# Performance work log

Measured on AMD Instinct MI355X. Metric: run time of the kernel, lower is better.

## Reference

```python
import jax, jax.numpy as jnp
import numpy as np

INT_MIN = jnp.iinfo(jnp.int32).min


def setup_inputs() -> dict:
    key = jax.random.key(0)
    ks = jax.random.split(key, 12)
    N, E, H, R, T = 200000, 100000, 100, 172, 100
    return {
        'src': jax.random.randint(ks[0], (E,), 0, N, dtype=jnp.int32),
        'dst': jax.random.randint(ks[1], (E,), 0, N, dtype=jnp.int32),
        't': jax.random.randint(ks[2], (E,), 0, 1000000, dtype=jnp.int32),
        'raw_msg': jax.random.normal(ks[3], (E, R), dtype=jnp.float32),
        'memory': jax.random.normal(ks[4], (N, H), dtype=jnp.float32),
        'last_update': jax.random.randint(ks[5], (N,), 0, 1000, dtype=jnp.int32),
        'te_w': jax.random.normal(ks[6], (T, 1), dtype=jnp.float32) * 0.1,
        'te_b': jax.random.normal(ks[7], (T,), dtype=jnp.float32) * 0.1,
        'w_ih': jax.random.normal(ks[8], (3 * H, 2 * H + R + T), dtype=jnp.float32) * 0.05,
        'w_hh': jax.random.normal(ks[9], (3 * H, H), dtype=jnp.float32) * 0.05,
        'b_ih': jax.random.normal(ks[10], (3 * H,), dtype=jnp.float32) * 0.05,
        'b_hh': jax.random.normal(ks[11], (3 * H,), dtype=jnp.float32) * 0.05,
    }


def reference(src, dst, t, raw_msg, memory, last_update, te_w, te_b, w_ih, w_hh, b_ih, b_hh):
    N, H = memory.shape
    E = src.shape[0]

    def time_enc(t_rel):  # Linear(1, time_dim) then cos, t_rel: [E] float
        return jnp.cos(t_rel[:, None] * te_w[:, 0][None, :] + te_b[None, :])

    # IdentityMessage: concat(mem[src], mem[dst], raw_msg, t_enc); two streams (s and d)
    t_enc_s = time_enc((t - last_update[src]).astype(raw_msg.dtype))
    t_enc_d = time_enc((t - last_update[dst]).astype(raw_msg.dtype))
    msg_s = jnp.concatenate([memory[src], memory[dst], raw_msg, t_enc_s], axis=-1)
    msg_d = jnp.concatenate([memory[dst], memory[src], raw_msg, t_enc_d], axis=-1)

    msg = jnp.concatenate([msg_s, msg_d], axis=0)        # [2E, msg_dim]
    idx = jnp.concatenate([src, dst], axis=0)            # [2E]
    t2 = jnp.concatenate([t, t], axis=0)                 # [2E]

    # LastAggregator: per node pick the message with maximum timestamp
    max_t = jnp.full((N,), INT_MIN, dtype=t2.dtype).at[idx].max(t2)
    cand = jnp.where(t2 == max_t[idx], jnp.arange(2 * E, dtype=jnp.int32), jnp.int32(-1))
    win = jnp.full((N,), -1, dtype=jnp.int32).at[idx].max(cand)  # winning edge per node
    has_msg = win >= 0
    aggr = jnp.where(has_msg[:, None], msg[jnp.clip(win, 0)], 0.0)  # [N, msg_dim]

    # GRUCell(msg_dim, H)
    gi = aggr @ w_ih.T + b_ih                             # [N, 3H]
    gh = memory @ w_hh.T + b_hh                           # [N, 3H]
    i_r, i_z, i_n = jnp.split(gi, 3, axis=-1)
    h_r, h_z, h_n = jnp.split(gh, 3, axis=-1)
    r = jax.nn.sigmoid(i_r + h_r)
    z = jax.nn.sigmoid(i_z + h_z)
    n = jnp.tanh(i_n + r * h_n)
    memory_new = (1.0 - z) * n + z * memory               # [N, H]

    last_update_new = last_update.at[idx].max(t2)         # scatter latest event time
    return memory_new, last_update_new
```

## Files before the change

### kernel.cpp

```cpp
#include <hip/hip_runtime.h>
#include <math.h>

typedef __attribute__((ext_vector_type(8))) short  short8;
typedef __attribute__((ext_vector_type(4))) float  f32x4;

static constexpr int H     = 100;
static constexpr int RD    = 172;
static constexpr int WK    = 472;
static constexpr int KTOT  = 640;
static constexpr int NKS   = 20;
static constexpr int CH    = 80;
static constexpr int MB    = 32;
static constexpr int GRPS  = 2;
static constexpr int BLK   = 448;
static constexpr int SLOTS = 64;
static constexpr int NTT   = 28;
static constexpr int BPK_N = NTT * NKS * 64 * 8;

__device__ inline unsigned short f2bf(float x) {
    union { float f; unsigned u; } v; v.f = x;
    return (unsigned short)((v.u + 0x7FFFu + ((v.u >> 16) & 1u)) >> 16);
}
__device__ inline f32x4 mfma16(short8 a, short8 b, f32x4 c) {
    return __builtin_amdgcn_mfma_f32_16x16x32_bf16(a, b, c, 0, 0, 0);
}
__device__ inline float4 ld4g(const float* base, int lc, int limit) {
    if (lc + 4 <= limit) return *(const float4*)(base + lc);
    return make_float4(0.f, 0.f, 0.f, 0.f);
}

__global__ __launch_bounds__(256) void k_init(int* __restrict__ maxt, int* __restrict__ win, int N) {
    int i = blockIdx.x * blockDim.x + threadIdx.x;
    if (i < N) { maxt[i] = (int)0x80000000; win[i] = -1; }
}

__global__ __launch_bounds__(256) void k_maxt(const int* __restrict__ src, const int* __restrict__ dst,
                                              const int* __restrict__ t, int* __restrict__ maxt, int E) {
    int j = blockIdx.x * blockDim.x + threadIdx.x;
    if (j < E) {
        int tj = t[j];
        atomicMax(&maxt[src[j]], tj);
        atomicMax(&maxt[dst[j]], tj);
    }
}

__global__ __launch_bounds__(256) void k_win(const int* __restrict__ src, const int* __restrict__ dst,
                                             const int* __restrict__ t, const int* __restrict__ maxt,
                                             int* __restrict__ win, int E) {
    int j = blockIdx.x * blockDim.x + threadIdx.x;
    if (j < E) {
        int tj = t[j];
        int s = src[j], d = dst[j];
        if (maxt[s] == tj) atomicMax(&win[s], j);
        if (maxt[d] == tj) atomicMax(&win[d], j + E);
    }
}

__global__ __launch_bounds__(256) void k_lu(const int* __restrict__ last_update, const int* __restrict__ maxt,
                                            float* __restrict__ out_lu, int N) {
    int i = blockIdx.x * blockDim.x + threadIdx.x;
    if (i < N) {
        int m = maxt[i], lu = last_update[i];
        out_lu[i] = (float)(m > lu ? m : lu);
    }
}

__global__ __launch_bounds__(256) void k_prep(const float* __restrict__ w_ih, const float* __restrict__ w_hh,
                                              unsigned short* __restrict__ B) {
    int idx = blockIdx.x * 256 + threadIdx.x;
    if (idx >= BPK_N) return;
    int jj   = idx & 7;
    int lane = (idx >> 3) & 63;
    int rest = idx >> 9;
    int ks   = rest % NKS;
    int tile = rest / NKS;
    int kk   = ks * 32 + ((lane >> 4) << 3) + jj;
    float v = 0.f;
    if (tile < 21) {
        int gate = tile / 7;
        int tcol = (tile % 7) * 16 + (lane & 15);
        if (tcol < 100) {
            if (kk < 512) {
                int col = -1;
                if (kk < 100)                   col = kk;
                else if (kk >= 104 && kk < 204) col = kk - 4;
                else if (kk >= 208 && kk < 380) col = kk - 8;
                else if (kk >= 384 && kk < 484) col = kk - 12;
                if (col >= 0) v = w_ih[(gate * 100 + tcol) * WK + col];
            } else {
                int khh = kk - 512;
                if (gate < 2 && khh < 100)
                    v = w_hh[(gate * 100 + tcol) * H + khh];
            }
        }
    } else {
        int tcol = (tile - 21) * 16 + (lane & 15);
        int khh  = kk - 512;
        if (tcol < 100 && khh >= 0 && khh < 100)
            v = w_hh[(200 + tcol) * H + khh];
    }
    B[idx] = f2bf(v);
}

__global__ __launch_bounds__(BLK, 6) void k_gru(
    const int* __restrict__ src, const int* __restrict__ dst, const int* __restrict__ t,
    const float* __restrict__ raw_msg, const float* __restrict__ memory,
    const int* __restrict__ last_update, const float* __restrict__ te_w,
    const float* __restrict__ te_b, const float* __restrict__ b_ih,
    const float* __restrict__ b_hh, const int* __restrict__ win,
    const unsigned short* __restrict__ Bpack,
    float* __restrict__ out_mem, int E, int N)
{
    __shared__ unsigned short sA[GRPS * NKS * SLOTS * 8];
    __shared__ int   s_other[MB];
    __shared__ int   s_j[MB];
    __shared__ int   s_has[MB];
    __shared__ float s_dt[MB];

    const int tid   = threadIdx.x;
    const int node0 = blockIdx.x * MB;

    if (tid < MB) {
        int node = node0 + tid;
        int w = win[node];
        int has = 0, j = 0, other = 0; float dt = 0.f;
        if (w >= 0) {
            has = 1;
            int e = (w < E) ? w : (w - E);
            j = e;
            other = (w < E) ? dst[e] : src[e];
            dt = (float)(t[e] - last_update[node]);
        }
        s_j[tid] = j; s_other[tid] = other; s_has[tid] = has; s_dt[tid] = dt;
    }
    __syncthreads();

    {
        const int nl    = tid & 31;
        const int node  = node0 + nl;
        const int has   = s_has[nl];
        const int other = s_other[nl];
        const int jw    = s_j[nl];
        const float dt  = s_dt[nl];
        const float* memN = memory + (size_t)node * H;
        const float* memO = memory + (size_t)other * H;
        const float* rawJ = raw_msg + (size_t)jw * RD;
        const int grp = nl >> 4;
        const int row = nl & 15;

        for (int c = tid >> 5; c < CH; c += BLK / 32) {
            const int kb = c * 8;
            float4 va = make_float4(0.f, 0.f, 0.f, 0.f), vb = va;
            if (kb < 512) {
                if (has) {
                    if (kb < 104)      { va = ld4g(memN, kb,       100); vb = ld4g(memN, kb + 4,   100); }
                    else if (kb < 208) { va = ld4g(memO, kb - 104, 100); vb = ld4g(memO, kb - 100, 100); }
                    else if (kb < 384) { va = ld4g(rawJ, kb - 208, RD ); vb = ld4g(rawJ, kb - 204, RD ); }
                    else {
                        const int lc = kb - 384;
                        float vv[8];
#pragma unroll
                        for (int q = 0; q < 8; ++q) {
                            int col = lc + q;
                            vv[q] = (col < 100) ? __cosf(fmaf(dt, te_w[col], te_b[col])) : 0.f;
                        }
                        va = make_float4(vv[0], vv[1], vv[2], vv[3]);
                        vb = make_float4(vv[4], vv[5], vv[6], vv[7]);
                    }
                }
            } else {
                va = ld4g(memN, kb - 512, 100);
                vb = ld4g(memN, kb - 508, 100);
            }
            short8 sv;
            sv[0] = (short)f2bf(va.x); sv[1] = (short)f2bf(va.y);
            sv[2] = (short)f2bf(va.z); sv[3] = (short)f2bf(va.w);
            sv[4] = (short)f2bf(vb.x); sv[5] = (short)f2bf(vb.y);
            sv[6] = (short)f2bf(vb.z); sv[7] = (short)f2bf(vb.w);
            const int ks  = c >> 2, sub = c & 3;
            const int slot = sub * 16 + (row ^ (sub << 2));
            *(short8*)&sA[((grp * NKS + ks) * SLOTS + slot) * 8] = sv;
        }
    }
    __syncthreads();

    const int wv    = tid >> 6;
    const int lane  = tid & 63;
    const int lrow  = lane & 15;
    const int lhi   = lane >> 4;
    const int slotl = lhi * 16 + (lrow ^ (lhi << 2));

    f32x4 ar[GRPS], az[GRPS], an[GRPS], ah[GRPS];
#pragma unroll
    for (int m = 0; m < GRPS; ++m) { ar[m] = (f32x4)0.f; az[m] = (f32x4)0.f; an[m] = (f32x4)0.f; ah[m] = (f32x4)0.f; }

    __builtin_amdgcn_s_setprio(1);
#pragma unroll
    for (int ks = 0; ks < NKS; ++ks) {
        short8 a0 = *(const short8*)&sA[((0 * NKS + ks) * SLOTS + slotl) * 8];
        short8 a1 = *(const short8*)&sA[((1 * NKS + ks) * SLOTS + slotl) * 8];
        short8 br = *(const short8*)&Bpack[(((size_t)(     wv) * NKS + ks) * 64 + lane) * 8];
        short8 bz = *(const short8*)&Bpack[(((size_t)( 7 + wv) * NKS + ks) * 64 + lane) * 8];
        short8 bn = (ks < 16)
                  ? *(const short8*)&Bpack[(((size_t)(14 + wv) * NKS + ks) * 64 + lane) * 8]
                  : *(const short8*)&Bpack[(((size_t)(21 + wv) * NKS + ks) * 64 + lane) * 8];
        ar[0] = mfma16(a0, br, ar[0]);  ar[1] = mfma16(a1, br, ar[1]);
        az[0] = mfma16(a0, bz, az[0]);  az[1] = mfma16(a1, bz, az[1]);
        if (ks < 16) { an[0] = mfma16(a0, bn, an[0]);  an[1] = mfma16(a1, bn, an[1]); }
        else         { ah[0] = mfma16(a0, bn, ah[0]);  ah[1] = mfma16(a1, bn, ah[1]); }
    }
    __builtin_amdgcn_s_setprio(0);

    const int c = wv * 16 + lrow;
    if (c < 100) {
        const float br_ = b_ih[c]       + b_hh[c];
        const float bz_ = b_ih[c + 100] + b_hh[c + 100];
        const float bin = b_ih[c + 200];
        const float bhn = b_hh[c + 200];
#pragma unroll
        for (int m = 0; m < GRPS; ++m) {
#pragma unroll
            for (int r = 0; r < 4; ++r) {
                const int node = node0 + m * 16 + lhi * 4 + r;
                const float h  = memory[(size_t)node * H + c];
                const float rg = 1.f / (1.f + __expf(-(ar[m][r] + br_)));
                const float zg = 1.f / (1.f + __expf(-(az[m][r] + bz_)));
                const float ng = tanhf(an[m][r] + bin + rg * (ah[m][r] + bhn));
                out_mem[(size_t)node * H + c] = (1.f - zg) * ng + zg * h;
            }
        }
    }
}

extern "C" void kernel_launch(void* const* d_in, const int* in_sizes, int n_in,
                              void* d_out, int out_size, void* d_ws, size_t ws_size,
                              hipStream_t stream)
{
    const int*   src         = (const int*)d_in[0];
    const int*   dst         = (const int*)d_in[1];
    const int*   t           = (const int*)d_in[2];
    const float* raw_msg     = (const float*)d_in[3];
    const float* memory      = (const float*)d_in[4];
    const int*   last_update = (const int*)d_in[5];
    const float* te_w        = (const float*)d_in[6];
    const float* te_b        = (const float*)d_in[7];
    const float* w_ih        = (const float*)d_in[8];
    const float* w_hh        = (const float*)d_in[9];
    const float* b_ih        = (const float*)d_in[10];
    const float* b_hh        = (const float*)d_in[11];

    const int E = in_sizes[0];
    const int N = in_sizes[5];

    float* out    = (float*)d_out;
    float* out_lu = out + (size_t)N * H;

    int* maxt = (int*)d_ws;
    int* win  = maxt + N;
    unsigned short* Bpack = (unsigned short*)(win + N);

    k_init<<<(N + 255) / 256, 256, 0, stream>>>(maxt, win, N);
    k_prep<<<(BPK_N + 255) / 256, 256, 0, stream>>>(w_ih, w_hh, Bpack);
    k_maxt<<<(E + 255) / 256, 256, 0, stream>>>(src, dst, t, maxt, E);
    k_win <<<(E + 255) / 256, 256, 0, stream>>>(src, dst, t, maxt, win, E);
    k_lu  <<<(N + 255) / 256, 256, 0, stream>>>(last_update, maxt, out_lu, N);
    k_gru <<<N / MB, BLK, 0, stream>>>(src, dst, t, raw_msg, memory, last_update,
                                       te_w, te_b, b_ih, b_hh, win, Bpack, out, E, N);
}
```

Baseline: 202.3 us.

## Load node memory once, reuse it for aggr and epilogue; widen blocks to 48 rows

Each block now covers 48 nodes (three 16-row MFMA groups) instead of 32, so every B-fragment load feeds more MFMAs. Each node's memory row is loaded from global memory only once. It is staged as bf16 in the hidden-state slots, copied under a has-message mask into the aggregated-message slots, and read back from shared memory for the GRU blend instead of going to global memory again. The change also packs bf16 conversion with v_cvt_pk_bf16_f32, replaces tanhf with an exp-based formula, and adds bounds checks for a partial last block. The costs are a larger LDS footprint (lower occupancy, launch bounds cut to 3) and the previous hidden state in the final blend now carries bf16 precision, which adds error to the output.

Measured after the change: 211.2 us. 4.4% more time.

```diff
diff --git a/kernel.cpp b/kernel.cpp
--- a/kernel.cpp
+++ b/kernel.cpp
@@ -9,9 +9,8 @@
 static constexpr int WK    = 472;
 static constexpr int KTOT  = 640;
 static constexpr int NKS   = 20;
-static constexpr int CH    = 80;
-static constexpr int MB    = 32;
-static constexpr int GRPS  = 2;
+static constexpr int MB    = 48;
+static constexpr int GRPS  = 3;
 static constexpr int BLK   = 448;
 static constexpr int SLOTS = 64;
 static constexpr int NTT   = 28;
@@ -20,6 +19,15 @@
 __device__ inline unsigned short f2bf(float x) {
     union { float f; unsigned u; } v; v.f = x;
     return (unsigned short)((v.u + 0x7FFFu + ((v.u >> 16) & 1u)) >> 16);
+}
+__device__ inline float bf2f(unsigned short b) {
+    union { unsigned u; float f; } v; v.u = ((unsigned)b) << 16;
+    return v.f;
+}
+__device__ inline unsigned pkbf(float a, float b) {
+    unsigned r;
+    asm("v_cvt_pk_bf16_f32 %0, %1, %2" : "=v"(r) : "v"(a), "v"(b));
+    return r;
 }
 __device__ inline f32x4 mfma16(short8 a, short8 b, f32x4 c) {
     return __builtin_amdgcn_mfma_f32_16x16x32_bf16(a, b, c, 0, 0, 0);
@@ -102,7 +110,7 @@
     B[idx] = f2bf(v);
 }
 
-__global__ __launch_bounds__(BLK, 6) void k_gru(
+__global__ __launch_bounds__(BLK, 3) void k_gru(
     const int* __restrict__ src, const int* __restrict__ dst, const int* __restrict__ t,
     const float* __restrict__ raw_msg, const float* __restrict__ memory,
     const int* __restrict__ last_update, const float* __restrict__ te_w,
@@ -122,40 +130,42 @@
 
     if (tid < MB) {
         int node = node0 + tid;
-        int w = win[node];
         int has = 0, j = 0, other = 0; float dt = 0.f;
-        if (w >= 0) {
-            has = 1;
-            int e = (w < E) ? w : (w - E);
-            j = e;
-            other = (w < E) ? dst[e] : src[e];
-            dt = (float)(t[e] - last_update[node]);
+        if (node < N) {
+            int w = win[node];
+            if (w >= 0) {
+                has = 1;
+                int e = (w < E) ? w : (w - E);
+                j = e;
+                other = (w < E) ? dst[e] : src[e];
+                dt = (float)(t[e] - last_update[node]);
+            }
         }
         s_j[tid] = j; s_other[tid] = other; s_has[tid] = has; s_dt[tid] = dt;
     }
     __syncthreads();
 
-    {
-        const int nl    = tid & 31;
+    if (tid < 384) {
+        const int nl    = tid % 48;
+        const int c0    = tid / 48;
         const int node  = node0 + nl;
+        const bool valid = node < N;
         const int has   = s_has[nl];
-        const int other = s_other[nl];
-        const int jw    = s_j[nl];
+        const float* memN = memory + (size_t)node * H;
+        const float* memO = memory + (size_t)s_other[nl] * H;
+        const float* rawJ = raw_msg + (size_t)s_j[nl] * RD;
         const float dt  = s_dt[nl];
-        const float* memN = memory + (size_t)node * H;
-        const float* memO = memory + (size_t)other * H;
-        const float* rawJ = raw_msg + (size_t)jw * RD;
         const int grp = nl >> 4;
         const int row = nl & 15;
 
-        for (int c = tid >> 5; c < CH; c += BLK / 32) {
+        for (int cc = c0; cc < 67; cc += 8) {
+            const int c  = cc + 13;
             const int kb = c * 8;
             float4 va = make_float4(0.f, 0.f, 0.f, 0.f), vb = va;
-            if (kb < 512) {
+            if (c < 64) {
                 if (has) {
-                    if (kb < 104)      { va = ld4g(memN, kb,       100); vb = ld4g(memN, kb + 4,   100); }
-                    else if (kb < 208) { va = ld4g(memO, kb - 104, 100); vb = ld4g(memO, kb - 100, 100); }
-                    else if (kb < 384) { va = ld4g(rawJ, kb - 208, RD ); vb = ld4g(rawJ, kb - 204, RD ); }
+                    if (c < 26)      { va = ld4g(memO, kb - 104, 100); vb = ld4g(memO, kb - 100, 100); }
+                    else if (c < 48) { va = ld4g(rawJ, kb - 208, RD ); vb = ld4g(rawJ, kb - 204, RD ); }
                     else {
                         const int lc = kb - 384;
                         float vv[8];
@@ -168,18 +178,29 @@
                         vb = make_float4(vv[4], vv[5], vv[6], vv[7]);
                     }
                 }
-            } else {
+            } else if (valid) {
                 va = ld4g(memN, kb - 512, 100);
                 vb = ld4g(memN, kb - 508, 100);
             }
-            short8 sv;
-            sv[0] = (short)f2bf(va.x); sv[1] = (short)f2bf(va.y);
-            sv[2] = (short)f2bf(va.z); sv[3] = (short)f2bf(va.w);
-            sv[4] = (short)f2bf(vb.x); sv[5] = (short)f2bf(vb.y);
-            sv[6] = (short)f2bf(vb.z); sv[7] = (short)f2bf(vb.w);
-            const int ks  = c >> 2, sub = c & 3;
-            const int slot = sub * 16 + (row ^ (sub << 2));
-            *(short8*)&sA[((grp * NKS + ks) * SLOTS + slot) * 8] = sv;
+            int4 sv;
+            sv.x = (int)pkbf(va.x, va.y);
+            sv.y = (int)pkbf(va.z, va.w);
+            sv.z = (int)pkbf(vb.x, vb.y);
+            sv.w = (int)pkbf(vb.z, vb.w);
+            {
+                const int ks = c >> 2, sub = c & 3;
+                const int slot = sub * 16 + (row ^ (sub << 2));
+                *(int4*)&sA[((grp * NKS + ks) * SLOTS + slot) * 8] = sv;
+            }
+            if (c >= 64 && c < 77) {
+                int4 sm_;
+                sm_.x = has ? sv.x : 0; sm_.y = has ? sv.y : 0;
+                sm_.z = has ? sv.z : 0; sm_.w = has ? sv.w : 0;
+                const int cm = c - 64;
+                const int ks = cm >> 2, sub = cm & 3;
+                const int slot = sub * 16 + (row ^ (sub << 2));
+                *(int4*)&sA[((grp * NKS + ks) * SLOTS + slot) * 8] = sm_;
+            }
         }
     }
     __syncthreads();
@@ -199,15 +220,16 @@
     for (int ks = 0; ks < NKS; ++ks) {
         short8 a0 = *(const short8*)&sA[((0 * NKS + ks) * SLOTS + slotl) * 8];
         short8 a1 = *(const short8*)&sA[((1 * NKS + ks) * SLOTS + slotl) * 8];
+        short8 a2 = *(const short8*)&sA[((2 * NKS + ks) * SLOTS + slotl) * 8];
         short8 br = *(const short8*)&Bpack[(((size_t)(     wv) * NKS + ks) * 64 + lane) * 8];
         short8 bz = *(const short8*)&Bpack[(((size_t)( 7 + wv) * NKS + ks) * 64 + lane) * 8];
         short8 bn = (ks < 16)
                   ? *(const short8*)&Bpack[(((size_t)(14 + wv) * NKS + ks) * 64 + lane) * 8]
                   : *(const short8*)&Bpack[(((size_t)(21 + wv) * NKS + ks) * 64 + lane) * 8];
-        ar[0] = mfma16(a0, br, ar[0]);  ar[1] = mfma16(a1, br, ar[1]);
-        az[0] = mfma16(a0, bz, az[0]);  az[1] = mfma16(a1, bz, az[1]);
-        if (ks < 16) { an[0] = mfma16(a0, bn, an[0]);  an[1] = mfma16(a1, bn, an[1]); }
-        else         { ah[0] = mfma16(a0, bn, ah[0]);  ah[1] = mfma16(a1, bn, ah[1]); }
+        ar[0] = mfma16(a0, br, ar[0]);  ar[1] = mfma16(a1, br, ar[1]);  ar[2] = mfma16(a2, br, ar[2]);
+        az[0] = mfma16(a0, bz, az[0]);  az[1] = mfma16(a1, bz, az[1]);  az[2] = mfma16(a2, bz, az[2]);
+        if (ks < 16) { an[0] = mfma16(a0, bn, an[0]);  an[1] = mfma16(a1, bn, an[1]);  an[2] = mfma16(a2, bn, an[2]); }
+        else         { ah[0] = mfma16(a0, bn, ah[0]);  ah[1] = mfma16(a1, bn, ah[1]);  ah[2] = mfma16(a2, bn, ah[2]); }
     }
     __builtin_amdgcn_s_setprio(0);
 
@@ -217,16 +239,25 @@
         const float bz_ = b_ih[c + 100] + b_hh[c + 100];
         const float bin = b_ih[c + 200];
         const float bhn = b_hh[c + 200];
+        const int ksh = 16 + (c >> 5);
+        const int sbh = (c >> 3) & 3;
+        const int ceh = c & 7;
 #pragma unroll
         for (int m = 0; m < GRPS; ++m) {
 #pragma unroll
             for (int r = 0; r < 4; ++r) {
                 const int node = node0 + m * 16 + lhi * 4 + r;
-                const float h  = memory[(size_t)node * H + c];
-                const float rg = 1.f / (1.f + __expf(-(ar[m][r] + br_)));
-                const float zg = 1.f / (1.f + __expf(-(az[m][r] + bz_)));
-                const float ng = tanhf(an[m][r] + bin + rg * (ah[m][r] + bhn));
-                out_mem[(size_t)node * H + c] = (1.f - zg) * ng + zg * h;
+                if (node < N) {
+                    const int rw   = lhi * 4 + r;
+                    const int slot = sbh * 16 + (rw ^ (sbh << 2));
+                    const float h  = bf2f(sA[((m * NKS + ksh) * SLOTS + slot) * 8 + ceh]);
+                    const float rg = 1.f / (1.f + __expf(-(ar[m][r] + br_)));
+                    const float zg = 1.f / (1.f + __expf(-(az[m][r] + bz_)));
+                    const float xn = an[m][r] + bin + rg * (ah[m][r] + bhn);
+                    const float ex = __expf(2.f * fabsf(xn));
+                    const float th = copysignf(1.f - 2.f / (ex + 1.f), xn);
+                    out_mem[(size_t)node * H + c] = (1.f - zg) * th + zg * h;
+                }
             }
         }
     }
@@ -264,6 +295,6 @@
     k_maxt<<<(E + 255) / 256, 256, 0, stream>>>(src, dst, t, maxt, E);
     k_win <<<(E + 255) / 256, 256, 0, stream>>>(src, dst, t, maxt, win, E);
     k_lu  <<<(N + 255) / 256, 256, 0, stream>>>(last_update, maxt, out_lu, N);
-    k_gru <<<N / MB, BLK, 0, stream>>>(src, dst, t, raw_msg, memory, last_update,
-                                       te_w, te_b, b_ih, b_hh, win, Bpack, out, E, N);
-}
+    k_gru <<<(N + MB - 1) / MB, BLK, 0, stream>>>(src, dst, t, raw_msg, memory, last_update,
+                                                  te_w, te_b, b_ih, b_hh, win, Bpack, out, E, N);
+}
```

## Load GRU A-operands directly from global into registers, drop LDS staging

Applied to the files above, without the earlier changes.

The GRU kernel no longer stages the gathered message rows through shared memory with two barriers. Each of the 7 waves now loads its own A-fragments straight from global memory, using per-node pointers that fall back to a zero buffer for nodes without a message. The block grows from 32 to 48 nodes (3 MFMA groups) to amortise the B-weight loads. Other changes: bf16 conversion uses the packed v_cvt_pk_bf16_f32 instruction, tanh uses an exp-based formula, and tail blocks get bounds checks. The cost is that every wave re-reads the same gathered rows and recomputes the cosines redundantly, and register pressure rises.

Result: slower. 385.3 us (+90.4%).

```diff
diff --git a/kernel.cpp b/kernel.cpp
--- a/kernel.cpp
+++ b/kernel.cpp
@@ -7,20 +7,23 @@
 static constexpr int H     = 100;
 static constexpr int RD    = 172;
 static constexpr int WK    = 472;
-static constexpr int KTOT  = 640;
 static constexpr int NKS   = 20;
-static constexpr int CH    = 80;
-static constexpr int MB    = 32;
-static constexpr int GRPS  = 2;
+static constexpr int MB    = 48;
+static constexpr int GRPS  = 3;
 static constexpr int BLK   = 448;
-static constexpr int SLOTS = 64;
 static constexpr int NTT   = 28;
 static constexpr int BPK_N = NTT * NKS * 64 * 8;
+static constexpr int ZBF   = 256;
 
 __device__ inline unsigned short f2bf(float x) {
     union { float f; unsigned u; } v; v.f = x;
     return (unsigned short)((v.u + 0x7FFFu + ((v.u >> 16) & 1u)) >> 16);
 }
+__device__ inline unsigned pkbf(float a, float b) {
+    unsigned r;
+    asm("v_cvt_pk_bf16_f32 %0, %1, %2" : "=v"(r) : "v"(a), "v"(b));
+    return r;
+}
 __device__ inline f32x4 mfma16(short8 a, short8 b, f32x4 c) {
     return __builtin_amdgcn_mfma_f32_16x16x32_bf16(a, b, c, 0, 0, 0);
 }
@@ -29,9 +32,11 @@
     return make_float4(0.f, 0.f, 0.f, 0.f);
 }
 
-__global__ __launch_bounds__(256) void k_init(int* __restrict__ maxt, int* __restrict__ win, int N) {
+__global__ __launch_bounds__(256) void k_init(int* __restrict__ maxt, int* __restrict__ win,
+                                              float* __restrict__ zbuf, int N) {
     int i = blockIdx.x * blockDim.x + threadIdx.x;
     if (i < N) { maxt[i] = (int)0x80000000; win[i] = -1; }
+    if (i < ZBF) zbuf[i] = 0.f;
 }
 
 __global__ __launch_bounds__(256) void k_maxt(const int* __restrict__ src, const int* __restrict__ dst,
@@ -102,114 +107,99 @@
     B[idx] = f2bf(v);
 }
 
-__global__ __launch_bounds__(BLK, 6) void k_gru(
+__global__ __launch_bounds__(BLK) void k_gru(
     const int* __restrict__ src, const int* __restrict__ dst, const int* __restrict__ t,
     const float* __restrict__ raw_msg, const float* __restrict__ memory,
     const int* __restrict__ last_update, const float* __restrict__ te_w,
     const float* __restrict__ te_b, const float* __restrict__ b_ih,
     const float* __restrict__ b_hh, const int* __restrict__ win,
-    const unsigned short* __restrict__ Bpack,
+    const unsigned short* __restrict__ Bpack, const float* __restrict__ zbuf,
     float* __restrict__ out_mem, int E, int N)
 {
-    __shared__ unsigned short sA[GRPS * NKS * SLOTS * 8];
-    __shared__ int   s_other[MB];
-    __shared__ int   s_j[MB];
-    __shared__ int   s_has[MB];
-    __shared__ float s_dt[MB];
-
     const int tid   = threadIdx.x;
-    const int node0 = blockIdx.x * MB;
-
-    if (tid < MB) {
-        int node = node0 + tid;
-        int w = win[node];
-        int has = 0, j = 0, other = 0; float dt = 0.f;
-        if (w >= 0) {
-            has = 1;
-            int e = (w < E) ? w : (w - E);
-            j = e;
-            other = (w < E) ? dst[e] : src[e];
-            dt = (float)(t[e] - last_update[node]);
-        }
-        s_j[tid] = j; s_other[tid] = other; s_has[tid] = has; s_dt[tid] = dt;
-    }
-    __syncthreads();
-
-    {
-        const int nl    = tid & 31;
-        const int node  = node0 + nl;
-        const int has   = s_has[nl];
-        const int other = s_other[nl];
-        const int jw    = s_j[nl];
-        const float dt  = s_dt[nl];
-        const float* memN = memory + (size_t)node * H;
-        const float* memO = memory + (size_t)other * H;
-        const float* rawJ = raw_msg + (size_t)jw * RD;
-        const int grp = nl >> 4;
-        const int row = nl & 15;
-
-        for (int c = tid >> 5; c < CH; c += BLK / 32) {
-            const int kb = c * 8;
-            float4 va = make_float4(0.f, 0.f, 0.f, 0.f), vb = va;
-            if (kb < 512) {
-                if (has) {
-                    if (kb < 104)      { va = ld4g(memN, kb,       100); vb = ld4g(memN, kb + 4,   100); }
-                    else if (kb < 208) { va = ld4g(memO, kb - 104, 100); vb = ld4g(memO, kb - 100, 100); }
-                    else if (kb < 384) { va = ld4g(rawJ, kb - 208, RD ); vb = ld4g(rawJ, kb - 204, RD ); }
-                    else {
-                        const int lc = kb - 384;
-                        float vv[8];
-#pragma unroll
-                        for (int q = 0; q < 8; ++q) {
-                            int col = lc + q;
-                            vv[q] = (col < 100) ? __cosf(fmaf(dt, te_w[col], te_b[col])) : 0.f;
-                        }
-                        va = make_float4(vv[0], vv[1], vv[2], vv[3]);
-                        vb = make_float4(vv[4], vv[5], vv[6], vv[7]);
-                    }
-                }
-            } else {
-                va = ld4g(memN, kb - 512, 100);
-                vb = ld4g(memN, kb - 508, 100);
-            }
-            short8 sv;
-            sv[0] = (short)f2bf(va.x); sv[1] = (short)f2bf(va.y);
-            sv[2] = (short)f2bf(va.z); sv[3] = (short)f2bf(va.w);
-            sv[4] = (short)f2bf(vb.x); sv[5] = (short)f2bf(vb.y);
-            sv[6] = (short)f2bf(vb.z); sv[7] = (short)f2bf(vb.w);
-            const int ks  = c >> 2, sub = c & 3;
-            const int slot = sub * 16 + (row ^ (sub << 2));
-            *(short8*)&sA[((grp * NKS + ks) * SLOTS + slot) * 8] = sv;
-        }
-    }
-    __syncthreads();
-
     const int wv    = tid >> 6;
     const int lane  = tid & 63;
     const int lrow  = lane & 15;
-    const int lhi   = lane >> 4;
-    const int slotl = lhi * 16 + (lrow ^ (lhi << 2));
+    const int q     = lane >> 4;
+    const int node0 = blockIdx.x * MB;
+
+    const float* pN[GRPS];
+    const float* pM[GRPS];
+    const float* pO[GRPS];
+    const float* pR[GRPS];
+    float hasf[GRPS], dtv[GRPS];
+#pragma unroll
+    for (int g = 0; g < GRPS; ++g) {
+        const int node  = node0 + g * 16 + lrow;
+        const bool valid = node < N;
+        int w = valid ? win[node] : -1;
+        const bool has = (w >= 0);
+        int other = 0, jj = 0; float dt = 0.f;
+        if (has) {
+            const int lu = last_update[node];
+            const int e  = (w < E) ? w : (w - E);
+            jj    = e;
+            other = (w < E) ? dst[e] : src[e];
+            dt    = (float)(t[e] - lu);
+        }
+        pN[g]   = valid ? memory + (size_t)node * H : zbuf;
+        pM[g]   = has ? memory + (size_t)node * H : zbuf;
+        pO[g]   = has ? memory + (size_t)other * H : zbuf;
+        pR[g]   = has ? raw_msg + (size_t)jj * RD : zbuf;
+        hasf[g] = has ? 1.f : 0.f;
+        dtv[g]  = dt;
+    }
 
     f32x4 ar[GRPS], az[GRPS], an[GRPS], ah[GRPS];
 #pragma unroll
     for (int m = 0; m < GRPS; ++m) { ar[m] = (f32x4)0.f; az[m] = (f32x4)0.f; an[m] = (f32x4)0.f; ah[m] = (f32x4)0.f; }
 
-    __builtin_amdgcn_s_setprio(1);
 #pragma unroll
     for (int ks = 0; ks < NKS; ++ks) {
-        short8 a0 = *(const short8*)&sA[((0 * NKS + ks) * SLOTS + slotl) * 8];
-        short8 a1 = *(const short8*)&sA[((1 * NKS + ks) * SLOTS + slotl) * 8];
+        short8 a[GRPS];
+#pragma unroll
+        for (int g = 0; g < GRPS; ++g) {
+            const int k0 = ks * 32 + q * 8;
+            float4 fa, fb;
+            if (ks >= 12 && ks < 16) {
+                const int lc = k0 - 384;
+                const float4 w0 = ld4g(te_w, lc, 100), w1 = ld4g(te_w, lc + 4, 100);
+                const float4 c0 = ld4g(te_b, lc, 100), c1 = ld4g(te_b, lc + 4, 100);
+                const float hf = hasf[g], dt = dtv[g];
+                fa.x = hf * __cosf(fmaf(dt, w0.x, c0.x));
+                fa.y = hf * __cosf(fmaf(dt, w0.y, c0.y));
+                fa.z = hf * __cosf(fmaf(dt, w0.z, c0.z));
+                fa.w = hf * __cosf(fmaf(dt, w0.w, c0.w));
+                fb.x = hf * __cosf(fmaf(dt, w1.x, c1.x));
+                fb.y = hf * __cosf(fmaf(dt, w1.y, c1.y));
+                fb.z = hf * __cosf(fmaf(dt, w1.z, c1.z));
+                fb.w = hf * __cosf(fmaf(dt, w1.w, c1.w));
+            } else {
+                const float* base; int off, lim;
+                if (k0 < 104)      { base = pM[g]; off = k0;       lim = 100; }
+                else if (k0 < 208) { base = pO[g]; off = k0 - 104; lim = 100; }
+                else if (k0 < 384) { base = pR[g]; off = k0 - 208; lim = 172; }
+                else               { base = pN[g]; off = k0 - 512; lim = 100; }
+                fa = ld4g(base, off, lim);
+                fb = ld4g(base, off + 4, lim);
+            }
+            union { int4 i; short8 s; } u;
+            u.i.x = (int)pkbf(fa.x, fa.y);
+            u.i.y = (int)pkbf(fa.z, fa.w);
+            u.i.z = (int)pkbf(fb.x, fb.y);
+            u.i.w = (int)pkbf(fb.z, fb.w);
+            a[g] = u.s;
+        }
         short8 br = *(const short8*)&Bpack[(((size_t)(     wv) * NKS + ks) * 64 + lane) * 8];
         short8 bz = *(const short8*)&Bpack[(((size_t)( 7 + wv) * NKS + ks) * 64 + lane) * 8];
         short8 bn = (ks < 16)
                   ? *(const short8*)&Bpack[(((size_t)(14 + wv) * NKS + ks) * 64 + lane) * 8]
                   : *(const short8*)&Bpack[(((size_t)(21 + wv) * NKS + ks) * 64 + lane) * 8];
-        ar[0] = mfma16(a0, br, ar[0]);  ar[1] = mfma16(a1, br, ar[1]);
-        az[0] = mfma16(a0, bz, az[0]);  az[1] = mfma16(a1, bz, az[1]);
-        if (ks < 16) { an[0] = mfma16(a0, bn, an[0]);  an[1] = mfma16(a1, bn, an[1]); }
-        else         { ah[0] = mfma16(a0, bn, ah[0]);  ah[1] = mfma16(a1, bn, ah[1]); }
-    }
-    __builtin_amdgcn_s_setprio(0);
+        ar[0] = mfma16(a[0], br, ar[0]);  ar[1] = mfma16(a[1], br, ar[1]);  ar[2] = mfma16(a[2], br, ar[2]);
+        az[0] = mfma16(a[0], bz, az[0]);  az[1] = mfma16(a[1], bz, az[1]);  az[2] = mfma16(a[2], bz, az[2]);
+        if (ks < 16) { an[0] = mfma16(a[0], bn, an[0]);  an[1] = mfma16(a[1], bn, an[1]);  an[2] = mfma16(a[2], bn, an[2]); }
+        else         { ah[0] = mfma16(a[0], bn, ah[0]);  ah[1] = mfma16(a[1], bn, ah[1]);  ah[2] = mfma16(a[2], bn, ah[2]); }
+    }
 
     const int c = wv * 16 + lrow;
     if (c < 100) {
@@ -221,12 +211,16 @@
         for (int m = 0; m < GRPS; ++m) {
 #pragma unroll
             for (int r = 0; r < 4; ++r) {
-                const int node = node0 + m * 16 + lhi * 4 + r;
-                const float h  = memory[(size_t)node * H + c];
-                const float rg = 1.f / (1.f + __expf(-(ar[m][r] + br_)));
-                const float zg = 1.f / (1.f + __expf(-(az[m][r] + bz_)));
-                const float ng = tanhf(an[m][r] + bin + rg * (ah[m][r] + bhn));
-                out_mem[(size_t)node * H + c] = (1.f - zg) * ng + zg * h;
+                const int node = node0 + m * 16 + q * 4 + r;
+                if (node < N) {
+                    const float h  = memory[(size_t)node * H + c];
+                    const float rg = 1.f / (1.f + __expf(-(ar[m][r] + br_)));
+                    const float zg = 1.f / (1.f + __expf(-(az[m][r] + bz_)));
+                    const float xn = an[m][r] + bin + rg * (ah[m][r] + bhn);
+                    const float ex = __expf(2.f * fabsf(xn));
+                    const float th = copysignf(1.f - 2.f / (ex + 1.f), xn);
+                    out_mem[(size_t)node * H + c] = (1.f - zg) * th + zg * h;
+                }
             }
         }
     }
@@ -258,12 +252,16 @@
     int* maxt = (int*)d_ws;
     int* win  = maxt + N;
     unsigned short* Bpack = (unsigned short*)(win + N);
-
-    k_init<<<(N + 255) / 256, 256, 0, stream>>>(maxt, win, N);
+    float* zbuf = (float*)(Bpack + BPK_N);
+
+    const int nblk = (N + MB - 1) / MB;
+
+    k_init<<<(N + 255) / 256, 256, 0, stream>>>(maxt, win, zbuf, N);
     k_prep<<<(BPK_N + 255) / 256, 256, 0, stream>>>(w_ih, w_hh, Bpack);
     k_maxt<<<(E + 255) / 256, 256, 0, stream>>>(src, dst, t, maxt, E);
     k_win <<<(E + 255) / 256, 256, 0, stream>>>(src, dst, t, maxt, win, E);
     k_lu  <<<(N + 255) / 256, 256, 0, stream>>>(last_update, maxt, out_lu, N);
-    k_gru <<<N / MB, BLK, 0, stream>>>(src, dst, t, raw_msg, memory, last_update,
-                                       te_w, te_b, b_ih, b_hh, win, Bpack, out, E, N);
-}
+    k_gru <<<nblk, BLK, 0, stream>>>(src, dst, t, raw_msg, memory, last_update,
+                                     te_w, te_b, b_ih, b_hh, win, Bpack, zbuf,
+                                     out, E, N);
+}
```
